# Optimization experiments

Measured on AMD Instinct MI355X. Metric: run time of the kernel, lower is better.

Reference implementation:

```python
import jax, jax.numpy as jnp
import numpy as np

B, T, D, H, R = 16, 2048, 512, 1024, 16


def setup_inputs() -> dict:
    key = jax.random.key(0)
    ks = jax.random.split(key, 8)
    s = lambda d: 1.0 / np.sqrt(d)
    return {
        "x": jax.random.normal(ks[0], (B, T, D), jnp.float32),
        "Wx": jax.random.normal(ks[1], (D, H), jnp.float32) * s(D),
        "Wh": jax.random.normal(ks[2], (H, H), jnp.float32) * s(H),
        "Wq": jax.random.normal(ks[3], (D, R), jnp.float32) * s(D),
        "Wk": jax.random.normal(ks[4], (D, R), jnp.float32) * s(D),
        "Wv": jax.random.normal(ks[5], (D, H), jnp.float32) * s(D),
        "Wd": jax.random.normal(ks[6], (D, 1), jnp.float32) * s(D),
        "b": jnp.zeros((H,), jnp.float32),
        "bd": jnp.ones((1,), jnp.float32),
    }


def reference(x, Wx, Wh, Wq, Wk, Wv, Wd, b, bd):
    """DREAM fast-weight RNN.

    Per step: decay lambda_t = sigmoid(x_t Wd + bd)  (B,1)
              F_t = lambda_t * F_{t-1} + v_t k_t^T   (B,H,R) outer-product memory
              r_t = F_t q_t                          (B,H)   fast-weight read
              h_t = tanh(x_t Wx + h_{t-1} Wh + r_t + b)
    """
    Bsz = x.shape[0]
    Hd, Rk = Wv.shape[1], Wq.shape[1]
    # Precompute all time-parallel projections once (big GEMMs outside the scan).
    q = jnp.einsum('btd,dr->btr', x, Wq)            # (B,T,R)
    k = jnp.einsum('btd,dr->btr', x, Wk)            # (B,T,R)
    v = jnp.einsum('btd,dh->bth', x, Wv)            # (B,T,H)
    lam = jax.nn.sigmoid(jnp.einsum('btd,do->bto', x, Wd) + bd)  # (B,T,1)
    xw = jnp.einsum('btd,dh->bth', x, Wx)           # (B,T,H)

    h0 = jnp.zeros((Bsz, Hd), x.dtype)
    F0 = jnp.zeros((Bsz, Hd, Rk), x.dtype)

    def step(carry, inp):
        h, F = carry
        q_t, k_t, v_t, lam_t, xw_t = inp
        F = lam_t[:, :, None] * F + v_t[:, :, None] * k_t[:, None, :]  # (B,H,R)
        read = jnp.einsum('bhr,br->bh', F, q_t)
        h = jnp.tanh(xw_t + h @ Wh + read + b)
        return (h, F), h

    # scan over time axis
    inps = (q.transpose(1, 0, 2), k.transpose(1, 0, 2), v.transpose(1, 0, 2),
            lam.transpose(1, 0, 2), xw.transpose(1, 0, 2))
    (h_fin, F_fin), hs = jax.lax.scan(step, (h0, F0), inps)
    output = hs.transpose(1, 0, 2)  # (B,T,H)
    return output, h_fin, F_fin
```

## Files before the change

kernel.cpp:

```cpp
#include <hip/hip_runtime.h>
#include <math.h>

#define Bc 16
#define Tc 2048
#define Dc 512
#define Hc 1024
#define Rc 16

__global__ __launch_bounds__(256) void gemm_fused(const float* __restrict__ X,
                                                  const float* __restrict__ Wx,
                                                  const float* __restrict__ Wv,
                                                  float* __restrict__ out0,
                                                  float* __restrict__ vout)
{
    __shared__ float As[16][128];
    __shared__ float Bs[16][128];
    const float* W = blockIdx.z ? Wv : Wx;
    float* out     = blockIdx.z ? vout : out0;
    const int tid = threadIdx.x;
    const int m0 = blockIdx.x * 128;
    const int n0 = blockIdx.y * 128;
    const int tx = tid & 15, ty = tid >> 4;
    const int ar = tid >> 1, ak = (tid & 1) * 8;
    const int br = tid >> 4, bn = (tid & 15) * 8;
    float acc[8][8] = {};
    for (int k0 = 0; k0 < 512; k0 += 16) {
        if (k0) __syncthreads();
        float4 a0 = *(const float4*)&X[(size_t)(m0 + ar) * 512 + k0 + ak];
        float4 a1 = *(const float4*)&X[(size_t)(m0 + ar) * 512 + k0 + ak + 4];
        float4 b0 = *(const float4*)&W[(size_t)(k0 + br) * 1024 + n0 + bn];
        float4 b1 = *(const float4*)&W[(size_t)(k0 + br) * 1024 + n0 + bn + 4];
        As[ak + 0][ar] = a0.x; As[ak + 1][ar] = a0.y;
        As[ak + 2][ar] = a0.z; As[ak + 3][ar] = a0.w;
        As[ak + 4][ar] = a1.x; As[ak + 5][ar] = a1.y;
        As[ak + 6][ar] = a1.z; As[ak + 7][ar] = a1.w;
        *(float4*)&Bs[br][bn]     = b0;
        *(float4*)&Bs[br][bn + 4] = b1;
        __syncthreads();
        #pragma unroll
        for (int kk = 0; kk < 16; ++kk) {
            float4 xa = *(const float4*)&As[kk][ty * 8];
            float4 xb = *(const float4*)&As[kk][ty * 8 + 4];
            float4 ya = *(const float4*)&Bs[kk][tx * 8];
            float4 yb = *(const float4*)&Bs[kk][tx * 8 + 4];
            float a[8] = {xa.x, xa.y, xa.z, xa.w, xb.x, xb.y, xb.z, xb.w};
            float b[8] = {ya.x, ya.y, ya.z, ya.w, yb.x, yb.y, yb.z, yb.w};
            #pragma unroll
            for (int i = 0; i < 8; ++i)
                #pragma unroll
                for (int j = 0; j < 8; ++j)
                    acc[i][j] += a[i] * b[j];
        }
    }
    #pragma unroll
    for (int i = 0; i < 8; ++i) {
        float4 r0, r1;
        r0.x = acc[i][0]; r0.y = acc[i][1]; r0.z = acc[i][2]; r0.w = acc[i][3];
        r1.x = acc[i][4]; r1.y = acc[i][5]; r1.z = acc[i][6]; r1.w = acc[i][7];
        float* op = &out[(size_t)(m0 + ty * 8 + i) * 1024 + n0 + tx * 8];
        *(float4*)op       = r0;
        *(float4*)(op + 4) = r1;
    }
}

__global__ __launch_bounds__(256) void qkl_kernel(const float* __restrict__ X,
    const float* __restrict__ Wq, const float* __restrict__ Wk,
    const float* __restrict__ Wd, const float* __restrict__ bd,
    float* __restrict__ q, float* __restrict__ k, float* __restrict__ lam)
{
    __shared__ float xs[8 * 512];
    const int tid = threadIdx.x;
    const size_t row0 = (size_t)blockIdx.x * 8;
    #pragma unroll
    for (int c = 0; c < 4; ++c) {
        int f = (c * 256 + tid) * 4;
        *(float4*)&xs[f] = *(const float4*)&X[row0 * 512 + f];
    }
    __syncthreads();
    for (int t = tid; t < 264; t += 256) {
        int r = t / 33, c = t - r * 33;
        const float* xr = &xs[r * 512];
        const float* Wp; int ldw;
        if (c < 16)      { Wp = Wq + c;        ldw = 16; }
        else if (c < 32) { Wp = Wk + (c - 16); ldw = 16; }
        else             { Wp = Wd;            ldw = 1;  }
        float s = 0.f;
        for (int kk = 0; kk < 512; ++kk) s += xr[kk] * Wp[(size_t)kk * ldw];
        if (c < 16)      q[(row0 + r) * 16 + c] = s;
        else if (c < 32) k[(row0 + r) * 16 + (c - 16)] = s;
        else             lam[row0 + r] = 1.f / (1.f + expf(-(s + bd[0])));
    }
}

__global__ __launch_bounds__(256, 1) void rec_fused(
    const float* __restrict__ Wh, const float* __restrict__ qg,
    const float* __restrict__ kg, const float* __restrict__ vg,
    const float* __restrict__ lamg, const float* __restrict__ bias,
    float* __restrict__ out0, float* __restrict__ hfin,
    float* __restrict__ Ffin, float* __restrict__ hbuf,
    int* __restrict__ xcc_tab)
{
    __shared__ float hs[2 * 1152];
    __shared__ float red2[2][256];
    __shared__ float pre_lds[2][64];
    __shared__ float F_lds[64][17];

    const int tid = threadIdx.x;
    const int bid = blockIdx.x;
    const int g = bid & 7, sl = bid >> 3;
    const int c0 = sl * 32;
    const int kp = tid >> 3;
    const int cu = tid & 7;
    const int wv = tid >> 6;

    const int my_xcc = __builtin_amdgcn_s_getreg(63508) & 0xF;
    if (tid == 0) {
        int val = my_xcc + 1;
        int* tp = xcc_tab + bid;
        asm volatile("global_store_dword %0, %1, off sc0 sc1"
                     :: "v"(tp), "v"(val) : "memory");
    }

    float wr[128];
    #pragma unroll
    for (int i = 0; i < 32; ++i) {
        float4 w4 = *(const float4*)&Wh[(size_t)(kp * 32 + i) * 1024 + c0 + cu * 4];
        wr[i * 4 + 0] = w4.x; wr[i * 4 + 1] = w4.y;
        wr[i * 4 + 2] = w4.z; wr[i * 4 + 3] = w4.w;
    }

    const int sb_ = tid >> 7;
    const int f   = (tid & 127) * 8;
    float* stage_base = &hs[sb_ * 1152 + (f >> 5) * 36 + (f & 31)];

    int fastf;
    {
        const int prod_bid = (f >> 5) * 8 + g;
        const int* tp = xcc_tab + prod_bid;
        int tv;
        for (;;) {
            asm volatile("global_load_dword %0, %1, off sc0 sc1\n\t"
                         "s_waitcnt vmcnt(0)"
                         : "=&v"(tv) : "v"(tp) : "memory");
            if (tv != -1) break;
        }
        fastf = ((tv - 1) == my_xcc) ? 1 : 0;
    }

    const int j64 = tid & 63;
    const int fb = j64 >> 5, fci = j64 & 31;
    const int bg = g * 2 + fb;
    const bool isScan = (tid >= 192);
    const bool isFin  = (tid < 64);

    float bias_r = 0.f, plam = 0.f, pv = 0.f, pxw = 0.f;
    float4 pq[4], pk4[4];
    if (isScan) {
        bias_r = bias[c0 + fci];
        #pragma unroll
        for (int r = 0; r < 16; ++r) F_lds[j64][r] = 0.f;
        const size_t row = (size_t)bg * Tc;
        plam = lamg[row];
        pv   = vg[row * Hc + c0 + fci];
        pxw  = out0[row * Hc + c0 + fci];
        const float* qp  = qg + row * 16;
        const float* kpp = kg + row * 16;
        #pragma unroll
        for (int r4 = 0; r4 < 4; ++r4) {
            pq[r4]  = *(const float4*)(qp + r4 * 4);
            pk4[r4] = *(const float4*)(kpp + r4 * 4);
        }
    }

    for (int t = 0; t < Tc; ++t) {
        const int buf = t & 1;
        float* h_rd = hbuf + (t & 1) * (16 * 1024) + g * 2048;
        float* h_wr = hbuf + ((t + 1) & 1) * (16 * 1024) + g * 2048;
        const float off_r = ((t >> 1) & 1) ? 4.0f : 0.0f;
        const float off_w = (((t + 1) >> 1) & 1) ? 4.0f : 0.0f;

        if (isScan) {
            float rd = 0.f;
            #pragma unroll
            for (int r4 = 0; r4 < 4; ++r4) {
                float f0 = F_lds[j64][r4 * 4 + 0];
                float f1 = F_lds[j64][r4 * 4 + 1];
                float f2 = F_lds[j64][r4 * 4 + 2];
                float f3 = F_lds[j64][r4 * 4 + 3];
                f0 = plam * f0 + pv * pk4[r4].x; rd += f0 * pq[r4].x;
                f1 = plam * f1 + pv * pk4[r4].y; rd += f1 * pq[r4].y;
                f2 = plam * f2 + pv * pk4[r4].z; rd += f2 * pq[r4].z;
                f3 = plam * f3 + pv * pk4[r4].w; rd += f3 * pq[r4].w;
                F_lds[j64][r4 * 4 + 0] = f0;
                F_lds[j64][r4 * 4 + 1] = f1;
                F_lds[j64][r4 * 4 + 2] = f2;
                F_lds[j64][r4 * 4 + 3] = f3;
            }
            pre_lds[buf][j64] = pxw + rd + bias_r;
            if (t == Tc - 1) {
                #pragma unroll
                for (int r = 0; r < 16; ++r)
                    Ffin[((size_t)bg * Hc + c0 + fci) * 16 + r] = F_lds[j64][r];
            } else {
                const size_t row = (size_t)bg * Tc + (t + 1);
                plam = lamg[row];
                pv   = vg[row * Hc + c0 + fci];
                pxw  = out0[row * Hc + c0 + fci];
                const float* qp  = qg + row * 16;
                const float* kpp = kg + row * 16;
                #pragma unroll
                for (int r4 = 0; r4 < 4; ++r4) {
                    pq[r4]  = *(const float4*)(qp + r4 * 4);
                    pk4[r4] = *(const float4*)(kpp + r4 * 4);
                }
            }
        }

        if (t > 0) {
            const float lo = off_r - 1.5f, hi = off_r + 1.5f;
            const float* p0 = h_rd + sb_ * 1024 + f;
            const float* p1 = p0 + 4;
            float4 r0, r1;
            int tries = 0;
            for (;;) {
                if (fastf) {
                    asm volatile(
                        "global_load_dwordx4 %0, %2, off sc0\n\t"
                        "global_load_dwordx4 %1, %3, off sc0\n\t"
                        "s_waitcnt vmcnt(0)"
                        : "=&v"(r0), "=&v"(r1)
                        : "v"(p0), "v"(p1) : "memory");
                } else {
                    asm volatile(
                        "global_load_dwordx4 %0, %2, off sc0 sc1\n\t"
                        "global_load_dwordx4 %1, %3, off sc0 sc1\n\t"
                        "s_waitcnt vmcnt(0)"
                        : "=&v"(r0), "=&v"(r1)
                        : "v"(p0), "v"(p1) : "memory");
                }
                bool ok = r0.x > lo && r0.x < hi && r0.y > lo && r0.y < hi
                       && r0.z > lo && r0.z < hi && r0.w > lo && r0.w < hi
                       && r1.x > lo && r1.x < hi && r1.y > lo && r1.y < hi
                       && r1.z > lo && r1.z < hi && r1.w > lo && r1.w < hi;
                if (ok) break;
                if (fastf && ++tries > 64) fastf = 0;
            }
            r0.x -= off_r; r0.y -= off_r; r0.z -= off_r; r0.w -= off_r;
            r1.x -= off_r; r1.y -= off_r; r1.z -= off_r; r1.w -= off_r;
            *(float4*)(stage_base)     = r0;
            *(float4*)(stage_base + 4) = r1;
        } else {
            float4 z = {0.f, 0.f, 0.f, 0.f};
            *(float4*)(stage_base)     = z;
            *(float4*)(stage_base + 4) = z;
        }
        __syncthreads();

        float acc[8];
        #pragma unroll
        for (int z = 0; z < 8; ++z) acc[z] = 0.f;
        #pragma unroll
        for (int bb = 0; bb < 2; ++bb) {
            const float* hb = &hs[bb * 1152 + kp * 36];
            #pragma unroll
            for (int i = 0; i < 8; ++i) {
                float4 h4 = *(const float4*)(hb + i * 4);
                #pragma unroll
                for (int j = 0; j < 4; ++j)
                    acc[j * 2 + bb] += h4.x * wr[(i * 4 + 0) * 4 + j]
                                     + h4.y * wr[(i * 4 + 1) * 4 + j]
                                     + h4.z * wr[(i * 4 + 2) * 4 + j]
                                     + h4.w * wr[(i * 4 + 3) * 4 + j];
            }
        }

        #pragma unroll
        for (int z = 0; z < 8; ++z) {
            float s = acc[z];
            s += __shfl_xor(s, 8);
            s += __shfl_xor(s, 16);
            s += __shfl_xor(s, 32);
            acc[z] = s;
        }
        if (j64 < 8) {
            float4 ra, rb;
            ra.x = acc[0]; ra.y = acc[1]; ra.z = acc[2]; ra.w = acc[3];
            rb.x = acc[4]; rb.y = acc[5]; rb.z = acc[6]; rb.w = acc[7];
            *(float4*)&red2[buf][wv * 64 + j64 * 8]     = ra;
            *(float4*)&red2[buf][wv * 64 + j64 * 8 + 4] = rb;
        }
        __syncthreads();

        if (isFin) {
            const int cu_f = fci >> 2, jf = fci & 3;
            const int z = jf * 2 + fb;
            float tot = pre_lds[buf][j64];
            #pragma unroll
            for (int ww = 0; ww < 4; ++ww)
                tot += red2[buf][ww * 64 + cu_f * 8 + z];
            float hv = tanhf(tot);
            float sv = hv + off_w;
            float* hp = h_wr + fb * 1024 + c0 + fci;
            asm volatile(
                "global_store_dword %0, %1, off sc0 sc1"
                :: "v"(hp), "v"(sv) : "memory");
            size_t oidx = ((size_t)bg * Tc + t) * Hc + c0 + fci;
            out0[oidx] = hv;
            if (t == Tc - 1) hfin[(size_t)bg * Hc + c0 + fci] = hv;
        }
    }
}

extern "C" void kernel_launch(void* const* d_in, const int* in_sizes, int n_in,
                              void* d_out, int out_size, void* d_ws, size_t ws_size,
                              hipStream_t stream)
{
    const float* x    = (const float*)d_in[0];
    const float* Wx   = (const float*)d_in[1];
    const float* Wh   = (const float*)d_in[2];
    const float* Wq   = (const float*)d_in[3];
    const float* Wk   = (const float*)d_in[4];
    const float* Wv   = (const float*)d_in[5];
    const float* Wd   = (const float*)d_in[6];
    const float* bias = (const float*)d_in[7];
    const float* bd   = (const float*)d_in[8];

    float* out0 = (float*)d_out;
    float* hfin = out0 + (size_t)Bc * Tc * Hc;
    float* Ffin = hfin + (size_t)Bc * Hc;

    float* wsf  = (float*)d_ws;
    float* v    = wsf;
    float* q    = v + (size_t)Bc * Tc * Hc;
    float* k    = q + (size_t)Bc * Tc * Rc;
    float* lam  = k + (size_t)Bc * Tc * Rc;
    float* hbuf = lam + (size_t)Bc * Tc;
    int*   xcc  = (int*)(hbuf + 2 * (size_t)Bc * Hc);

    hipMemsetAsync(hbuf, 0x7F, 2 * (size_t)Bc * Hc * sizeof(float), stream);
    hipMemsetAsync(xcc, 0xFF, 256 * sizeof(int), stream);

    dim3 gp(256, 8, 2);
    gemm_fused<<<gp, 256, 0, stream>>>(x, Wx, Wv, out0, v);
    qkl_kernel<<<4096, 256, 0, stream>>>(x, Wq, Wk, Wd, bd, q, k, lam);
    rec_fused<<<256, 256, 0, stream>>>(Wh, q, k, v, lam, bias,
                                       out0, hfin, Ffin, hbuf, xcc);
}
```

Measured before the change: 7.536 ms.

## Restructure recurrent kernel so each wave owns full dot products without LDS barriers

Each wave now handles one batch row and 8 output columns. Its 64 lanes cover the full K=1024 with 16 Wh rows each held in registers, so the matvec is reduced across the wave with shuffles. This removes the LDS staging of h, the cross-wave reduction buffers and both __syncthreads per timestep. The fast-weight state F also moves from LDS into registers. In exchange every wave polls and reads the entire 4 KB h row from global memory each step, which is 4x more duplicated traffic, and the shuffle reduction is longer. Blocks grow to 512 threads.

After: 11.23 ms. +49.0%, slower.

```diff
diff --git a/kernel.cpp b/kernel.cpp
--- a/kernel.cpp
+++ b/kernel.cpp
@@ -92,7 +92,7 @@
     }
 }
 
-__global__ __launch_bounds__(256, 1) void rec_fused(
+__global__ __launch_bounds__(512, 2) void rec_fused(
     const float* __restrict__ Wh, const float* __restrict__ qg,
     const float* __restrict__ kg, const float* __restrict__ vg,
     const float* __restrict__ lamg, const float* __restrict__ bias,
@@ -100,18 +100,13 @@
     float* __restrict__ Ffin, float* __restrict__ hbuf,
     int* __restrict__ xcc_tab)
 {
-    __shared__ float hs[2 * 1152];
-    __shared__ float red2[2][256];
-    __shared__ float pre_lds[2][64];
-    __shared__ float F_lds[64][17];
-
     const int tid = threadIdx.x;
     const int bid = blockIdx.x;
-    const int g = bid & 7, sl = bid >> 3;
-    const int c0 = sl * 32;
-    const int kp = tid >> 3;
-    const int cu = tid & 7;
-    const int wv = tid >> 6;
+    const int g = bid & 7, s = bid >> 3;
+    const int w = tid >> 6;
+    const int lane = tid & 63;
+    const int bg = g * 2 + (w >> 2);
+    const int c0 = (s * 4 + (w & 3)) * 8;
 
     const int my_xcc = __builtin_amdgcn_s_getreg(63508) & 0xF;
     if (tid == 0) {
@@ -123,46 +118,47 @@
 
     float wr[128];
     #pragma unroll
-    for (int i = 0; i < 32; ++i) {
-        float4 w4 = *(const float4*)&Wh[(size_t)(kp * 32 + i) * 1024 + c0 + cu * 4];
-        wr[i * 4 + 0] = w4.x; wr[i * 4 + 1] = w4.y;
-        wr[i * 4 + 2] = w4.z; wr[i * 4 + 3] = w4.w;
-    }
-
-    const int sb_ = tid >> 7;
-    const int f   = (tid & 127) * 8;
-    float* stage_base = &hs[sb_ * 1152 + (f >> 5) * 36 + (f & 31)];
+    for (int i = 0; i < 16; ++i) {
+        const float* wp = &Wh[(size_t)(lane * 16 + i) * 1024 + c0];
+        float4 wa = *(const float4*)wp;
+        float4 wb = *(const float4*)(wp + 4);
+        wr[i * 8 + 0] = wa.x; wr[i * 8 + 1] = wa.y;
+        wr[i * 8 + 2] = wa.z; wr[i * 8 + 3] = wa.w;
+        wr[i * 8 + 4] = wb.x; wr[i * 8 + 5] = wb.y;
+        wr[i * 8 + 6] = wb.z; wr[i * 8 + 7] = wb.w;
+    }
 
     int fastf;
     {
-        const int prod_bid = (f >> 5) * 8 + g;
-        const int* tp = xcc_tab + prod_bid;
+        const int* tp = xcc_tab + ((lane >> 1) * 8 + g);
         int tv;
         for (;;) {
             asm volatile("global_load_dword %0, %1, off sc0 sc1\n\t"
                          "s_waitcnt vmcnt(0)"
                          : "=&v"(tv) : "v"(tp) : "memory");
-            if (tv != -1) break;
+            if (__all(tv != -1)) break;
+            __builtin_amdgcn_s_sleep(1);
         }
         fastf = ((tv - 1) == my_xcc) ? 1 : 0;
     }
 
-    const int j64 = tid & 63;
-    const int fb = j64 >> 5, fci = j64 & 31;
-    const int bg = g * 2 + fb;
-    const bool isScan = (tid >= 192);
-    const bool isFin  = (tid < 64);
-
+    const bool isScan = (lane < 8);
+    float F[16];
+    #pragma unroll
+    for (int r = 0; r < 16; ++r) F[r] = 0.f;
     float bias_r = 0.f, plam = 0.f, pv = 0.f, pxw = 0.f;
     float4 pq[4], pk4[4];
+    #pragma unroll
+    for (int r4 = 0; r4 < 4; ++r4) {
+        pq[r4]  = make_float4(0.f, 0.f, 0.f, 0.f);
+        pk4[r4] = make_float4(0.f, 0.f, 0.f, 0.f);
+    }
     if (isScan) {
-        bias_r = bias[c0 + fci];
-        #pragma unroll
-        for (int r = 0; r < 16; ++r) F_lds[j64][r] = 0.f;
+        bias_r = bias[c0 + lane];
         const size_t row = (size_t)bg * Tc;
         plam = lamg[row];
-        pv   = vg[row * Hc + c0 + fci];
-        pxw  = out0[row * Hc + c0 + fci];
+        pv   = vg[row * Hc + c0 + lane];
+        pxw  = out0[row * Hc + c0 + lane];
         const float* qp  = qg + row * 16;
         const float* kpp = kg + row * 16;
         #pragma unroll
@@ -173,39 +169,35 @@
     }
 
     for (int t = 0; t < Tc; ++t) {
-        const int buf = t & 1;
-        float* h_rd = hbuf + (t & 1) * (16 * 1024) + g * 2048;
-        float* h_wr = hbuf + ((t + 1) & 1) * (16 * 1024) + g * 2048;
+        float* h_rd = hbuf + (t & 1) * (16 * 1024) + bg * 1024;
+        float* h_wr = hbuf + ((t + 1) & 1) * (16 * 1024) + bg * 1024;
         const float off_r = ((t >> 1) & 1) ? 4.0f : 0.0f;
         const float off_w = (((t + 1) >> 1) & 1) ? 4.0f : 0.0f;
 
+        float pre_val = 0.f;
         if (isScan) {
             float rd = 0.f;
             #pragma unroll
             for (int r4 = 0; r4 < 4; ++r4) {
-                float f0 = F_lds[j64][r4 * 4 + 0];
-                float f1 = F_lds[j64][r4 * 4 + 1];
-                float f2 = F_lds[j64][r4 * 4 + 2];
-                float f3 = F_lds[j64][r4 * 4 + 3];
+                float f0 = F[r4 * 4 + 0], f1 = F[r4 * 4 + 1];
+                float f2 = F[r4 * 4 + 2], f3 = F[r4 * 4 + 3];
                 f0 = plam * f0 + pv * pk4[r4].x; rd += f0 * pq[r4].x;
                 f1 = plam * f1 + pv * pk4[r4].y; rd += f1 * pq[r4].y;
                 f2 = plam * f2 + pv * pk4[r4].z; rd += f2 * pq[r4].z;
                 f3 = plam * f3 + pv * pk4[r4].w; rd += f3 * pq[r4].w;
-                F_lds[j64][r4 * 4 + 0] = f0;
-                F_lds[j64][r4 * 4 + 1] = f1;
-                F_lds[j64][r4 * 4 + 2] = f2;
-                F_lds[j64][r4 * 4 + 3] = f3;
+                F[r4 * 4 + 0] = f0; F[r4 * 4 + 1] = f1;
+                F[r4 * 4 + 2] = f2; F[r4 * 4 + 3] = f3;
             }
-            pre_lds[buf][j64] = pxw + rd + bias_r;
+            pre_val = pxw + rd + bias_r;
             if (t == Tc - 1) {
                 #pragma unroll
                 for (int r = 0; r < 16; ++r)
-                    Ffin[((size_t)bg * Hc + c0 + fci) * 16 + r] = F_lds[j64][r];
+                    Ffin[((size_t)bg * Hc + c0 + lane) * 16 + r] = F[r];
             } else {
                 const size_t row = (size_t)bg * Tc + (t + 1);
                 plam = lamg[row];
-                pv   = vg[row * Hc + c0 + fci];
-                pxw  = out0[row * Hc + c0 + fci];
+                pv   = vg[row * Hc + c0 + lane];
+                pxw  = out0[row * Hc + c0 + lane];
                 const float* qp  = qg + row * 16;
                 const float* kpp = kg + row * 16;
                 #pragma unroll
@@ -216,97 +208,87 @@
             }
         }
 
+        float4 r0, r1, r2, r3;
         if (t > 0) {
             const float lo = off_r - 1.5f, hi = off_r + 1.5f;
-            const float* p0 = h_rd + sb_ * 1024 + f;
-            const float* p1 = p0 + 4;
-            float4 r0, r1;
+            const float* p0 = h_rd + lane * 16;
             int tries = 0;
             for (;;) {
                 if (fastf) {
                     asm volatile(
-                        "global_load_dwordx4 %0, %2, off sc0\n\t"
-                        "global_load_dwordx4 %1, %3, off sc0\n\t"
+                        "global_load_dwordx4 %0, %4, off sc0\n\t"
+                        "global_load_dwordx4 %1, %4, off offset:16 sc0\n\t"
+                        "global_load_dwordx4 %2, %4, off offset:32 sc0\n\t"
+                        "global_load_dwordx4 %3, %4, off offset:48 sc0\n\t"
                         "s_waitcnt vmcnt(0)"
-                        : "=&v"(r0), "=&v"(r1)
-                        : "v"(p0), "v"(p1) : "memory");
+                        : "=&v"(r0), "=&v"(r1), "=&v"(r2), "=&v"(r3)
+                        : "v"(p0) : "memory");
                 } else {
                     asm volatile(
-                        "global_load_dwordx4 %0, %2, off sc0 sc1\n\t"
-                        "global_load_dwordx4 %1, %3, off sc0 sc1\n\t"
+                        "global_load_dwordx4 %0, %4, off sc0 sc1\n\t"
+                        "global_load_dwordx4 %1, %4, off offset:16 sc0 sc1\n\t"
+                        "global_load_dwordx4 %2, %4, off offset:32 sc0 sc1\n\t"
+                        "global_load_dwordx4 %3, %4, off offset:48 sc0 sc1\n\t"
                         "s_waitcnt vmcnt(0)"
-                        : "=&v"(r0), "=&v"(r1)
-                        : "v"(p0), "v"(p1) : "memory");
+                        : "=&v"(r0), "=&v"(r1), "=&v"(r2), "=&v"(r3)
+                        : "v"(p0) : "memory");
                 }
                 bool ok = r0.x > lo && r0.x < hi && r0.y > lo && r0.y < hi
                        && r0.z > lo && r0.z < hi && r0.w > lo && r0.w < hi
                        && r1.x > lo && r1.x < hi && r1.y > lo && r1.y < hi
-                       && r1.z > lo && r1.z < hi && r1.w > lo && r1.w < hi;
+                       && r1.z > lo && r1.z < hi && r1.w > lo && r1.w < hi
+                       && r2.x > lo && r2.x < hi && r2.y > lo && r2.y < hi
+                       && r2.z > lo && r2.z < hi && r2.w > lo && r2.w < hi
+                       && r3.x > lo && r3.x < hi && r3.y > lo && r3.y < hi
+                       && r3.z > lo && r3.z < hi && r3.w > lo && r3.w < hi;
                 if (ok) break;
                 if (fastf && ++tries > 64) fastf = 0;
             }
             r0.x -= off_r; r0.y -= off_r; r0.z -= off_r; r0.w -= off_r;
             r1.x -= off_r; r1.y -= off_r; r1.z -= off_r; r1.w -= off_r;
-            *(float4*)(stage_base)     = r0;
-            *(float4*)(stage_base + 4) = r1;
+            r2.x -= off_r; r2.y -= off_r; r2.z -= off_r; r2.w -= off_r;
+            r3.x -= off_r; r3.y -= off_r; r3.z -= off_r; r3.w -= off_r;
         } else {
-            float4 z = {0.f, 0.f, 0.f, 0.f};
-            *(float4*)(stage_base)     = z;
-            *(float4*)(stage_base + 4) = z;
-        }
-        __syncthreads();
+            r0 = make_float4(0.f, 0.f, 0.f, 0.f);
+            r1 = r0; r2 = r0; r3 = r0;
+        }
 
         float acc[8];
         #pragma unroll
-        for (int z = 0; z < 8; ++z) acc[z] = 0.f;
-        #pragma unroll
-        for (int bb = 0; bb < 2; ++bb) {
-            const float* hb = &hs[bb * 1152 + kp * 36];
+        for (int c = 0; c < 8; ++c) acc[c] = 0.f;
+        const float hv16[16] = {r0.x, r0.y, r0.z, r0.w, r1.x, r1.y, r1.z, r1.w,
+                                r2.x, r2.y, r2.z, r2.w, r3.x, r3.y, r3.z, r3.w};
+        #pragma unroll
+        for (int i = 0; i < 16; ++i)
             #pragma unroll
-            for (int i = 0; i < 8; ++i) {
-                float4 h4 = *(const float4*)(hb + i * 4);
-                #pragma unroll
-                for (int j = 0; j < 4; ++j)
-                    acc[j * 2 + bb] += h4.x * wr[(i * 4 + 0) * 4 + j]
-                                     + h4.y * wr[(i * 4 + 1) * 4 + j]
-                                     + h4.z * wr[(i * 4 + 2) * 4 + j]
-                                     + h4.w * wr[(i * 4 + 3) * 4 + j];
-            }
-        }
-
-        #pragma unroll
-        for (int z = 0; z < 8; ++z) {
-            float s = acc[z];
-            s += __shfl_xor(s, 8);
-            s += __shfl_xor(s, 16);
-            s += __shfl_xor(s, 32);
-            acc[z] = s;
-        }
-        if (j64 < 8) {
-            float4 ra, rb;
-            ra.x = acc[0]; ra.y = acc[1]; ra.z = acc[2]; ra.w = acc[3];
-            rb.x = acc[4]; rb.y = acc[5]; rb.z = acc[6]; rb.w = acc[7];
-            *(float4*)&red2[buf][wv * 64 + j64 * 8]     = ra;
-            *(float4*)&red2[buf][wv * 64 + j64 * 8 + 4] = rb;
-        }
-        __syncthreads();
-
-        if (isFin) {
-            const int cu_f = fci >> 2, jf = fci & 3;
-            const int z = jf * 2 + fb;
-            float tot = pre_lds[buf][j64];
+            for (int c = 0; c < 8; ++c)
+                acc[c] += hv16[i] * wr[i * 8 + c];
+
+        #pragma unroll
+        for (int c = 0; c < 8; ++c) {
+            float sum = acc[c];
+            sum += __shfl_xor(sum, 1);
+            sum += __shfl_xor(sum, 2);
+            sum += __shfl_xor(sum, 4);
+            sum += __shfl_xor(sum, 8);
+            sum += __shfl_xor(sum, 16);
+            sum += __shfl_xor(sum, 32);
+            acc[c] = sum;
+        }
+
+        if (isScan) {
+            float hvv = 0.f;
             #pragma unroll
-            for (int ww = 0; ww < 4; ++ww)
-                tot += red2[buf][ww * 64 + cu_f * 8 + z];
-            float hv = tanhf(tot);
+            for (int c = 0; c < 8; ++c)
+                if (lane == c) hvv = acc[c];
+            float hv = tanhf(hvv + pre_val);
             float sv = hv + off_w;
-            float* hp = h_wr + fb * 1024 + c0 + fci;
-            asm volatile(
-                "global_store_dword %0, %1, off sc0 sc1"
-                :: "v"(hp), "v"(sv) : "memory");
-            size_t oidx = ((size_t)bg * Tc + t) * Hc + c0 + fci;
+            float* hp = h_wr + c0 + lane;
+            asm volatile("global_store_dword %0, %1, off sc0 sc1"
+                         :: "v"(hp), "v"(sv) : "memory");
+            size_t oidx = ((size_t)bg * Tc + t) * Hc + c0 + lane;
             out0[oidx] = hv;
-            if (t == Tc - 1) hfin[(size_t)bg * Hc + c0 + fci] = hv;
+            if (t == Tc - 1) hfin[(size_t)bg * Hc + c0 + lane] = hv;
         }
     }
 }
@@ -343,6 +325,6 @@
     dim3 gp(256, 8, 2);
     gemm_fused<<<gp, 256, 0, stream>>>(x, Wx, Wv, out0, v);
     qkl_kernel<<<4096, 256, 0, stream>>>(x, Wq, Wk, Wd, bd, q, k, lam);
-    rec_fused<<<256, 256, 0, stream>>>(Wh, q, k, v, lam, bias,
+    rec_fused<<<256, 512, 0, stream>>>(Wh, q, k, v, lam, bias,
                                        out0, hfin, Ffin, hbuf, xcc);
 }
```
